# Kernel optimization log

Measured on AMD Instinct MI355X. Metric: run time of the kernel, lower is better.

## Reference

```python
import jax, jax.numpy as jnp
import numpy as np

OVERLAP_THRESHOLD = 0.5
NEG_POS_RATIO = 3
ALPHA = 1.0


def cxcy_to_xy(cxcy):
    return jnp.concatenate([cxcy[..., :2] - cxcy[..., 2:] / 2,
                            cxcy[..., :2] + cxcy[..., 2:] / 2], axis=-1)


def xy_to_cxcy(xy):
    return jnp.concatenate([(xy[..., :2] + xy[..., 2:]) / 2,
                            xy[..., 2:] - xy[..., :2]], axis=-1)


def cxcy_to_gcxgcy(cxcy, priors_cxcy):
    return jnp.concatenate([
        (cxcy[..., :2] - priors_cxcy[..., :2]) / (priors_cxcy[..., 2:] / 10.0),
        jnp.log(cxcy[..., 2:] / priors_cxcy[..., 2:]) * 5.0], axis=-1)


def jaccard(a, b):
    # a: [N,4] xy, b: [P,4] xy -> [N,P]
    lo = jnp.maximum(a[:, None, :2], b[None, :, :2])
    hi = jnp.minimum(a[:, None, 2:], b[None, :, 2:])
    inter = jnp.prod(jnp.clip(hi - lo, 0.0), axis=-1)  # [N,P]
    area_a = jnp.prod(a[:, 2:] - a[:, :2], axis=-1)  # [N]
    area_b = jnp.prod(b[:, 2:] - b[:, :2], axis=-1)  # [P]
    return inter / (area_a[:, None] + area_b[None, :] - inter)


def _match_one(boxes_i, labels_i, priors_cxcy, priors_xy):
    n_objects = boxes_i.shape[0]
    overlap = jaccard(boxes_i, priors_xy)  # [N,P]
    overlap_for_each_prior = overlap.max(axis=0)  # [P]
    object_for_each_prior = overlap.argmax(axis=0)  # [P]
    prior_for_each_object = overlap.argmax(axis=1)  # [N]
    # force each object to own its best prior
    object_for_each_prior = object_for_each_prior.at[prior_for_each_object].set(
        jnp.arange(n_objects))
    overlap_for_each_prior = overlap_for_each_prior.at[prior_for_each_object].set(1.0)
    labels_for_each_prior = labels_i[object_for_each_prior]
    labels_for_each_prior = jnp.where(overlap_for_each_prior < OVERLAP_THRESHOLD,
                                      0, labels_for_each_prior)
    matched = boxes_i[object_for_each_prior]  # [P,4]
    true_locs = cxcy_to_gcxgcy(xy_to_cxcy(matched), priors_cxcy)  # [P,4]
    return true_locs, labels_for_each_prior


def reference(predicted_locs, predicted_scores, boxes, labels, priors_cxcy):
    B, P, C = predicted_scores.shape
    priors_xy = cxcy_to_xy(priors_cxcy)
    true_locs, true_classes = jax.vmap(
        _match_one, in_axes=(0, 0, None, None))(boxes, labels, priors_cxcy, priors_xy)
    # true_locs: [B,P,4], true_classes: [B,P]
    positive = true_classes != 0  # [B,P]
    n_pos = positive.sum(axis=1)  # [B]
    n_pos_total = n_pos.sum()

    # SmoothL1 (beta=1, mean over selected elements = n_pos_total*4)
    d = predicted_locs - true_locs
    ad = jnp.abs(d)
    sl1 = jnp.where(ad < 1.0, 0.5 * d * d, ad - 0.5)  # [B,P,4]
    loc_loss = (sl1 * positive[..., None]).sum() / (n_pos_total.astype(jnp.float32) * 4.0)

    # per-prior cross-entropy
    logp = jax.nn.log_softmax(predicted_scores, axis=-1)  # [B,P,C]
    conf_all = -jnp.take_along_axis(logp, true_classes[..., None], axis=-1)[..., 0]  # [B,P]

    conf_pos_sum = jnp.where(positive, conf_all, 0.0).sum()
    conf_neg = jnp.where(positive, 0.0, conf_all)
    conf_neg_sorted = jnp.sort(conf_neg, axis=1)[:, ::-1]  # descending
    n_hard_neg = NEG_POS_RATIO * n_pos  # [B]
    rank = jnp.arange(P)[None, :]
    hard_neg_mask = rank < n_hard_neg[:, None]
    conf_hard_neg_sum = jnp.where(hard_neg_mask, conf_neg_sorted, 0.0).sum()

    conf_loss = (conf_hard_neg_sum + conf_pos_sum) / n_pos_total.astype(jnp.float32)
    return conf_loss + ALPHA * loc_loss


def setup_inputs() -> dict:
    key = jax.random.key(0)
    ks = jax.random.split(key, 7)
    B, P, C, N = 128, 8732, 21, 16
    predicted_locs = jax.random.normal(ks[0], (B, P, 4), dtype=jnp.float32)
    predicted_scores = jax.random.normal(ks[1], (B, P, C), dtype=jnp.float32)
    # valid xy boxes in [0,1]
    p1 = jax.random.uniform(ks[2], (B, N, 2)) * 0.85
    wh = jax.random.uniform(ks[3], (B, N, 2), minval=0.02, maxval=0.15)
    boxes = jnp.concatenate([p1, jnp.minimum(p1 + wh, 1.0)], axis=-1)
    labels = jax.random.randint(ks[4], (B, N), 1, C)
    cxcy = jax.random.uniform(ks[5], (P, 2))
    pwh = jax.random.uniform(ks[6], (P, 2), minval=0.05, maxval=0.5)
    priors_cxcy = jnp.concatenate([cxcy, pwh], axis=-1)
    return {"predicted_locs": predicted_locs, "predicted_scores": predicted_scores,
            "boxes": boxes, "labels": labels, "priors_cxcy": priors_cxcy}
```

## Files before the change

### kernel.cpp

```cpp
#include <hip/hip_runtime.h>


#define MAXN 16
#define MAXE 16

__device__ __forceinline__ float sl1f(float d) {
    float ad = fabsf(d);
    return ad < 1.0f ? 0.5f * d * d : ad - 0.5f;
}

__global__ __launch_bounds__(256) void k_bestprior(
    const float* __restrict__ boxes,
    const float* __restrict__ priors,
    int P, int N,
    int* __restrict__ pfo,
    int* __restrict__ npos)
{
    __shared__ float rv[4];
    __shared__ int   riq[4];
    const int id = blockIdx.x;
    const int tid = threadIdx.x;
    const int lane = tid & 63, wid = tid >> 6;

    if (tid == 0 && (id % N) == 0) npos[id / N] = 0;

    const float* bp = boxes + (size_t)id * 4;
    const float bx1 = bp[0], by1 = bp[1], bx2 = bp[2], by2 = bp[3];
    const float ba = (bx2 - bx1) * (by2 - by1);

    float v = -1.0f; int i = 0x7fffffff;
#pragma unroll 2
    for (int p = tid; p < P; p += 256) {
        float4 pr = ((const float4*)priors)[p];
        float px1 = pr.x - pr.z * 0.5f, py1 = pr.y - pr.w * 0.5f;
        float px2 = pr.x + pr.z * 0.5f, py2 = pr.y + pr.w * 0.5f;
        float parea = (px2 - px1) * (py2 - py1);
        float iw = fmaxf(fminf(bx2, px2) - fmaxf(bx1, px1), 0.0f);
        float ih = fmaxf(fminf(by2, py2) - fmaxf(by1, py1), 0.0f);
        float inter = iw * ih;
        float iou = inter / (ba + parea - inter);
        if (iou > v) { v = iou; i = p; }
    }
#pragma unroll
    for (int off = 32; off > 0; off >>= 1) {
        float ov = __shfl_down(v, off);
        int   oi = __shfl_down(i, off);
        if (ov > v || (ov == v && oi < i)) { v = ov; i = oi; }
    }
    if (lane == 0) { rv[wid] = v; riq[wid] = i; }
    __syncthreads();
    if (tid == 0) {
        for (int w = 1; w < 4; w++) {
            float ov = rv[w]; int oi = riq[w];
            if (ov > v || (ov == v && oi < i)) { v = ov; i = oi; }
        }
        pfo[id] = i;
    }
}

__global__ __launch_bounds__(256) void k_fused(
    const float* __restrict__ plocs,
    const float* __restrict__ scores,
    const float* __restrict__ boxes,
    const int*   __restrict__ labels,
    const float* __restrict__ priors,
    const int*   __restrict__ pfo,
    int P, int C, int N, int nchunk,
    float* __restrict__ conf_out,
    int*   __restrict__ npos,
    float* __restrict__ locpart,
    float* __restrict__ pospart)
{
    extern __shared__ float sh[];
    __shared__ float sx1[MAXN], sy1[MAXN], sx2[MAXN], sy2[MAXN], barea[MAXN];
    __shared__ int   blab[MAXN], spfo[MAXN];
    __shared__ float redf[4], redp[4];
    __shared__ int   redi[4];

    const int b = blockIdx.y;
    const int tid = threadIdx.x;
    const int lane = tid & 63, wid = tid >> 6;
    if (N > MAXN) N = MAXN;
    const int p0 = blockIdx.x * 256;
    const int rows = min(256, P - p0);

    if (tid < N) {
        const float* bp = boxes + ((size_t)b * N + tid) * 4;
        float x1 = bp[0], y1 = bp[1], x2 = bp[2], y2 = bp[3];
        sx1[tid] = x1; sy1[tid] = y1; sx2[tid] = x2; sy2[tid] = y2;
        barea[tid] = (x2 - x1) * (y2 - y1);
        blab[tid] = labels[(size_t)b * N + tid];
        spfo[tid] = pfo[b * N + tid];
    }

    {
        const size_t f4base = ((size_t)b * P + p0) * C / 4;
        const int f4cnt = (rows * C + 3) / 4;
        const float4* __restrict__ s4 = (const float4*)scores;
        for (int j = tid; j < f4cnt; j += 256)
            ((float4*)sh)[j] = s4[f4base + j];
    }
    __syncthreads();

    const int p = p0 + tid;
    float locs = 0.0f, posc = 0.0f, conf = 0.0f;
    int np = 0;
    if (p < P) {
        float4 pr = ((const float4*)priors)[p];
        float px1 = pr.x - pr.z * 0.5f, py1 = pr.y - pr.w * 0.5f;
        float px2 = pr.x + pr.z * 0.5f, py2 = pr.y + pr.w * 0.5f;
        float parea = (px2 - px1) * (py2 - py1);
        float best = -1.0f; int bestn = 0;
#pragma unroll
        for (int n = 0; n < MAXN; n++) {
            if (n < N) {
                float iw = fmaxf(fminf(sx2[n], px2) - fmaxf(sx1[n], px1), 0.0f);
                float ih = fmaxf(fminf(sy2[n], py2) - fmaxf(sy1[n], py1), 0.0f);
                float inter = iw * ih;
                float iou = inter / (barea[n] + parea - inter);
                if (iou > best) { best = iou; bestn = n; }
            }
        }
#pragma unroll
        for (int n = 0; n < MAXN; n++) {
            if (n < N && spfo[n] == p) { bestn = n; best = 1.0f; }
        }
        const int lab = (best < 0.5f) ? 0 : blab[bestn];

        const float* r = sh + tid * C;
        float m = -3.402823466e38f;
        for (int c = 0; c < C; c++) m = fmaxf(m, r[c]);
        float sum = 0.0f;
        for (int c = 0; c < C; c++) sum += __expf(r[c] - m);
        float ce = m + __logf(sum) - r[lab];

        if (lab != 0) {
            posc = ce; np = 1;
            int n = bestn;
            float cx = (sx1[n] + sx2[n]) * 0.5f, cy = (sy1[n] + sy2[n]) * 0.5f;
            float w = sx2[n] - sx1[n], h = sy2[n] - sy1[n];
            float g0 = (cx - pr.x) / (pr.z / 10.0f);
            float g1 = (cy - pr.y) / (pr.w / 10.0f);
            float g2 = logf(w / pr.z) * 5.0f;
            float g3 = logf(h / pr.w) * 5.0f;
            float4 pl = ((const float4*)plocs)[(size_t)b * P + p];
            locs = sl1f(pl.x - g0) + sl1f(pl.y - g1) + sl1f(pl.z - g2) + sl1f(pl.w - g3);
        } else {
            conf = ce;
        }
        conf_out[(size_t)b * P + p] = conf;
    }
#pragma unroll
    for (int off = 32; off > 0; off >>= 1) {
        locs += __shfl_down(locs, off);
        posc += __shfl_down(posc, off);
        np   += __shfl_down(np, off);
    }
    if (lane == 0) { redf[wid] = locs; redp[wid] = posc; redi[wid] = np; }
    __syncthreads();
    if (tid == 0) {
        float L = redf[0] + redf[1] + redf[2] + redf[3];
        float Pp = redp[0] + redp[1] + redp[2] + redp[3];
        int   c = redi[0] + redi[1] + redi[2] + redi[3];
        if (c) atomicAdd(&npos[b], c);
        locpart[b * nchunk + blockIdx.x] = L;
        pospart[b * nchunk + blockIdx.x] = Pp;
    }
}

__global__ __launch_bounds__(1024, 4) void k_hard(
    const float* __restrict__ conf,
    const int* __restrict__ npos,
    int P,
    float* __restrict__ hardsum)
{
    __shared__ int   redi[16 * 3];
    __shared__ float redf2[16];
    __shared__ int   redi2[16];
    const int b = blockIdx.x, tid = threadIdx.x;
    const int lane = tid & 63, wid = tid >> 6;
    const int nthr = blockDim.x, nw = nthr >> 6;
    const int ne = (P + nthr - 1) / nthr;
    long long kk = (long long)npos[b] * 3;
    int k = kk > P ? P : (int)kk;
    if (k <= 0) {
        if (tid == 0) hardsum[b] = 0.0f;
        return;
    }

    unsigned e[MAXE];
#pragma unroll
    for (int j = 0; j < MAXE; j++) {
        int p = j * nthr + tid;
        e[j] = (j < ne && p < P) ? __float_as_uint(conf[(size_t)b * P + p]) : 0u;
    }

    unsigned lo = 0u, hi = 0x7F800000u;
    while (lo < hi) {
        unsigned span = hi - lo;
        if (span >= 8) {
            unsigned q = span >> 2;
            unsigned m1 = lo + q, m2 = lo + 2 * q, m3 = lo + 3 * q;
            int c1 = 0, c2 = 0, c3 = 0;
#pragma unroll
            for (int j = 0; j < MAXE; j++) {
                if (j < ne) {
                    unsigned v = e[j];
                    c1 += (int)__popcll(__ballot(v >= m1));
                    c2 += (int)__popcll(__ballot(v >= m2));
                    c3 += (int)__popcll(__ballot(v >= m3));
                }
            }
            if (lane == 0) {
                redi[wid * 3 + 0] = c1; redi[wid * 3 + 1] = c2; redi[wid * 3 + 2] = c3;
            }
            __syncthreads();
            int C1 = 0, C2 = 0, C3 = 0;
            for (int w = 0; w < nw; w++) {
                C1 += redi[w * 3 + 0]; C2 += redi[w * 3 + 1]; C3 += redi[w * 3 + 2];
            }
            __syncthreads();
            if      (C3 >= k) lo = m3;
            else if (C2 >= k) { lo = m2; hi = m3 - 1; }
            else if (C1 >= k) { lo = m1; hi = m2 - 1; }
            else              hi = m1 - 1;
        } else {
            unsigned mid = lo + ((span + 1) >> 1);
            int c = 0;
#pragma unroll
            for (int j = 0; j < MAXE; j++)
                if (j < ne) c += (int)__popcll(__ballot(e[j] >= mid));
            if (lane == 0) redi[wid * 3] = c;
            __syncthreads();
            int Cc = 0;
            for (int w = 0; w < nw; w++) Cc += redi[w * 3];
            __syncthreads();
            if (Cc >= k) lo = mid; else hi = mid - 1;
        }
    }

    float t = __uint_as_float(lo);
    float sgt = 0.0f; int cgt = 0;
#pragma unroll
    for (int j = 0; j < MAXE; j++) {
        if (j < ne) {
            float v = __uint_as_float(e[j]);
            if (v > t) { sgt += v; cgt++; }
        }
    }
#pragma unroll
    for (int off = 32; off > 0; off >>= 1) {
        sgt += __shfl_down(sgt, off);
        cgt += __shfl_down(cgt, off);
    }
    if (lane == 0) { redf2[wid] = sgt; redi2[wid] = cgt; }
    __syncthreads();
    if (tid == 0) {
        float S = 0.0f; int Cg = 0;
        for (int w = 0; w < nw; w++) { S += redf2[w]; Cg += redi2[w]; }
        hardsum[b] = S + (float)(k - Cg) * t;
    }
}

__global__ __launch_bounds__(1024) void k_final(
    const int* __restrict__ npos, const float* __restrict__ locpart,
    const float* __restrict__ pospart, const float* __restrict__ hardsum,
    int B, int nloc, float* __restrict__ out)
{
    const int tid = threadIdx.x, lane = tid & 63, wid = tid >> 6;
    __shared__ float rf[3 * 16];
    __shared__ int   ri[16];
    float lp = 0, pp = 0, hp = 0; int np = 0;
    for (int i = tid; i < B; i += 1024) { np += npos[i]; hp += hardsum[i]; }
    for (int i = tid; i < nloc; i += 1024) { lp += locpart[i]; pp += pospart[i]; }
#pragma unroll
    for (int off = 32; off > 0; off >>= 1) {
        np += __shfl_down(np, off); lp += __shfl_down(lp, off);
        pp += __shfl_down(pp, off); hp += __shfl_down(hp, off);
    }
    if (lane == 0) { ri[wid] = np; rf[wid] = lp; rf[16 + wid] = pp; rf[32 + wid] = hp; }
    __syncthreads();
    if (tid == 0) {
        int nw = (int)(blockDim.x >> 6);
        float L = 0, Pp = 0, H = 0; int Np = 0;
        for (int w = 0; w < nw; w++) { Np += ri[w]; L += rf[w]; Pp += rf[16 + w]; H += rf[32 + w]; }
        float npf = (float)Np;
        out[0] = (H + Pp) / npf + L / (npf * 4.0f);
    }
}

extern "C" void kernel_launch(void* const* d_in, const int* in_sizes, int n_in,
                              void* d_out, int out_size, void* d_ws, size_t ws_size,
                              hipStream_t stream)
{
    const float* plocs  = (const float*)d_in[0];
    const float* scores = (const float*)d_in[1];
    const float* boxes  = (const float*)d_in[2];
    const int*   labels = (const int*)d_in[3];
    const float* priors = (const float*)d_in[4];

    int P = in_sizes[4] / 4;
    int B = in_sizes[0] / (P * 4);
    int C = in_sizes[1] / (in_sizes[0] / 4);
    int N = in_sizes[3] / B;
    int nchunk = (P + 255) / 256;
    int BN = B * N;

    char* w = (char*)d_ws;
    float* slot    = (float*)w;  w += (size_t)B * P * sizeof(float);
    int*   npos    = (int*)w;    w += (size_t)B * sizeof(int);
    int*   pfo     = (int*)w;    w += (size_t)BN * sizeof(int);
    float* locpart = (float*)w;  w += (size_t)B * nchunk * sizeof(float);
    float* pospart = (float*)w;  w += (size_t)B * nchunk * sizeof(float);
    float* hardsum = (float*)w;

    k_bestprior<<<BN, 256, 0, stream>>>(boxes, priors, P, N, pfo, npos);

    dim3 ga(nchunk, B);
    size_t smf = (size_t)256 * C * sizeof(float);
    k_fused<<<ga, 256, smf, stream>>>(plocs, scores, boxes, labels, priors, pfo,
                                      P, C, N, nchunk, slot, npos, locpart, pospart);

    k_hard<<<B, 1024, 0, stream>>>(slot, npos, P, hardsum);

    k_final<<<1, 1024, 0, stream>>>(npos, locpart, pospart, hardsum,
                                    B, B * nchunk, (float*)d_out);
}
```

Measured before the change: 221.4 us.

## Fold final reduction into hard-negative kernel via atomics; divide-free IoU comparisons

Removes the separate final reduction kernel. The fused kernel now atomically accumulates loc, positive-conf and positive-count totals into a small accumulator. The last block of the hard-negative kernel, detected with a ticket counter, computes the output. IoU argmax comparisons are rewritten as cross-multiplication to avoid divisions. This saves one launch and the divides, but adds about 4.4k float atomics on two addresses, which may contend, and gives nondeterministic summation order.

```diff
diff --git a/kernel.cpp b/kernel.cpp
--- a/kernel.cpp
+++ b/kernel.cpp
@@ -9,26 +9,28 @@
     return ad < 1.0f ? 0.5f * d * d : ad - 0.5f;
 }
 
-__global__ __launch_bounds__(256) void k_bestprior(
+__global__ __launch_bounds__(256) void k_pre(
     const float* __restrict__ boxes,
     const float* __restrict__ priors,
     int P, int N,
     int* __restrict__ pfo,
-    int* __restrict__ npos)
+    int* __restrict__ npos,
+    float* __restrict__ acc)
 {
-    __shared__ float rv[4];
-    __shared__ int   riq[4];
+    __shared__ float rin[4], run[4];
+    __shared__ int   rid[4];
     const int id = blockIdx.x;
     const int tid = threadIdx.x;
     const int lane = tid & 63, wid = tid >> 6;
 
     if (tid == 0 && (id % N) == 0) npos[id / N] = 0;
+    if (id == 0 && tid < 8) ((unsigned*)acc)[tid] = 0u;
 
     const float* bp = boxes + (size_t)id * 4;
     const float bx1 = bp[0], by1 = bp[1], bx2 = bp[2], by2 = bp[3];
     const float ba = (bx2 - bx1) * (by2 - by1);
 
-    float v = -1.0f; int i = 0x7fffffff;
+    float bi = -1.0f, bu = 1.0f; int idx = 0x7fffffff;
 #pragma unroll 2
     for (int p = tid; p < P; p += 256) {
         float4 pr = ((const float4*)priors)[p];
@@ -37,24 +39,27 @@
         float parea = (px2 - px1) * (py2 - py1);
         float iw = fmaxf(fminf(bx2, px2) - fmaxf(bx1, px1), 0.0f);
         float ih = fmaxf(fminf(by2, py2) - fmaxf(by1, py1), 0.0f);
-        float inter = iw * ih;
-        float iou = inter / (ba + parea - inter);
-        if (iou > v) { v = iou; i = p; }
+        float in = iw * ih;
+        float un = ba + parea - in;
+        if (in * bu > bi * un) { bi = in; bu = un; idx = p; }
     }
 #pragma unroll
     for (int off = 32; off > 0; off >>= 1) {
-        float ov = __shfl_down(v, off);
-        int   oi = __shfl_down(i, off);
-        if (ov > v || (ov == v && oi < i)) { v = ov; i = oi; }
-    }
-    if (lane == 0) { rv[wid] = v; riq[wid] = i; }
+        float oin = __shfl_down(bi, off);
+        float oun = __shfl_down(bu, off);
+        int   oid = __shfl_down(idx, off);
+        float a = oin * bu, c = bi * oun;
+        if (a > c || (a == c && oid < idx)) { bi = oin; bu = oun; idx = oid; }
+    }
+    if (lane == 0) { rin[wid] = bi; run[wid] = bu; rid[wid] = idx; }
     __syncthreads();
     if (tid == 0) {
         for (int w = 1; w < 4; w++) {
-            float ov = rv[w]; int oi = riq[w];
-            if (ov > v || (ov == v && oi < i)) { v = ov; i = oi; }
-        }
-        pfo[id] = i;
+            float oin = rin[w], oun = run[w]; int oid = rid[w];
+            float a = oin * bu, c = bi * oun;
+            if (a > c || (a == c && oid < idx)) { bi = oin; bu = oun; idx = oid; }
+        }
+        pfo[id] = idx;
     }
 }
 
@@ -65,11 +70,10 @@
     const int*   __restrict__ labels,
     const float* __restrict__ priors,
     const int*   __restrict__ pfo,
-    int P, int C, int N, int nchunk,
+    int P, int C, int N,
     float* __restrict__ conf_out,
     int*   __restrict__ npos,
-    float* __restrict__ locpart,
-    float* __restrict__ pospart)
+    float* __restrict__ acc)
 {
     extern __shared__ float sh[];
     __shared__ float sx1[MAXN], sy1[MAXN], sx2[MAXN], sy2[MAXN], barea[MAXN];
@@ -110,22 +114,22 @@
         float px1 = pr.x - pr.z * 0.5f, py1 = pr.y - pr.w * 0.5f;
         float px2 = pr.x + pr.z * 0.5f, py2 = pr.y + pr.w * 0.5f;
         float parea = (px2 - px1) * (py2 - py1);
-        float best = -1.0f; int bestn = 0;
+        float bi = -1.0f, bu = 1.0f; int bestn = 0;
 #pragma unroll
         for (int n = 0; n < MAXN; n++) {
             if (n < N) {
                 float iw = fmaxf(fminf(sx2[n], px2) - fmaxf(sx1[n], px1), 0.0f);
                 float ih = fmaxf(fminf(sy2[n], py2) - fmaxf(sy1[n], py1), 0.0f);
-                float inter = iw * ih;
-                float iou = inter / (barea[n] + parea - inter);
-                if (iou > best) { best = iou; bestn = n; }
+                float in = iw * ih;
+                float un = barea[n] + parea - in;
+                if (in * bu > bi * un) { bi = in; bu = un; bestn = n; }
             }
         }
 #pragma unroll
         for (int n = 0; n < MAXN; n++) {
-            if (n < N && spfo[n] == p) { bestn = n; best = 1.0f; }
-        }
-        const int lab = (best < 0.5f) ? 0 : blab[bestn];
+            if (n < N && spfo[n] == p) { bestn = n; bi = 1.0f; bu = 1.0f; }
+        }
+        const int lab = (bi < 0.5f * bu) ? 0 : blab[bestn];
 
         const float* r = sh + tid * C;
         float m = -3.402823466e38f;
@@ -162,9 +166,12 @@
         float L = redf[0] + redf[1] + redf[2] + redf[3];
         float Pp = redp[0] + redp[1] + redp[2] + redp[3];
         int   c = redi[0] + redi[1] + redi[2] + redi[3];
-        if (c) atomicAdd(&npos[b], c);
-        locpart[b * nchunk + blockIdx.x] = L;
-        pospart[b * nchunk + blockIdx.x] = Pp;
+        atomicAdd(&acc[0], L);
+        atomicAdd(&acc[1], Pp);
+        if (c) {
+            atomicAdd(&npos[b], c);
+            atomicAdd((int*)(acc + 3), c);
+        }
     }
 }
 
@@ -172,7 +179,8 @@
     const float* __restrict__ conf,
     const int* __restrict__ npos,
     int P,
-    float* __restrict__ hardsum)
+    float* __restrict__ acc,
+    float* __restrict__ out)
 {
     __shared__ int   redi[16 * 3];
     __shared__ float redf2[16];
@@ -183,109 +191,95 @@
     const int ne = (P + nthr - 1) / nthr;
     long long kk = (long long)npos[b] * 3;
     int k = kk > P ? P : (int)kk;
-    if (k <= 0) {
-        if (tid == 0) hardsum[b] = 0.0f;
-        return;
-    }
-
-    unsigned e[MAXE];
-#pragma unroll
-    for (int j = 0; j < MAXE; j++) {
-        int p = j * nthr + tid;
-        e[j] = (j < ne && p < P) ? __float_as_uint(conf[(size_t)b * P + p]) : 0u;
-    }
-
-    unsigned lo = 0u, hi = 0x7F800000u;
-    while (lo < hi) {
-        unsigned span = hi - lo;
-        if (span >= 8) {
-            unsigned q = span >> 2;
-            unsigned m1 = lo + q, m2 = lo + 2 * q, m3 = lo + 3 * q;
-            int c1 = 0, c2 = 0, c3 = 0;
-#pragma unroll
-            for (int j = 0; j < MAXE; j++) {
-                if (j < ne) {
-                    unsigned v = e[j];
-                    c1 += (int)__popcll(__ballot(v >= m1));
-                    c2 += (int)__popcll(__ballot(v >= m2));
-                    c3 += (int)__popcll(__ballot(v >= m3));
+
+    float S = 0.0f;
+    if (k > 0) {
+        unsigned e[MAXE];
+#pragma unroll
+        for (int j = 0; j < MAXE; j++) {
+            int p = j * nthr + tid;
+            e[j] = (j < ne && p < P) ? __float_as_uint(conf[(size_t)b * P + p]) : 0u;
+        }
+
+        unsigned lo = 0u, hi = 0x7F800000u;
+        while (lo < hi) {
+            unsigned span = hi - lo;
+            if (span >= 8) {
+                unsigned q = span >> 2;
+                unsigned m1 = lo + q, m2 = lo + 2 * q, m3 = lo + 3 * q;
+                int c1 = 0, c2 = 0, c3 = 0;
+#pragma unroll
+                for (int j = 0; j < MAXE; j++) {
+                    if (j < ne) {
+                        unsigned v = e[j];
+                        c1 += (int)__popcll(__ballot(v >= m1));
+                        c2 += (int)__popcll(__ballot(v >= m2));
+                        c3 += (int)__popcll(__ballot(v >= m3));
+                    }
                 }
+                if (lane == 0) {
+                    redi[wid * 3 + 0] = c1; redi[wid * 3 + 1] = c2; redi[wid * 3 + 2] = c3;
+                }
+                __syncthreads();
+                int C1 = 0, C2 = 0, C3 = 0;
+                for (int w = 0; w < nw; w++) {
+                    C1 += redi[w * 3 + 0]; C2 += redi[w * 3 + 1]; C3 += redi[w * 3 + 2];
+                }
+                __syncthreads();
+                if      (C3 >= k) lo = m3;
+                else if (C2 >= k) { lo = m2; hi = m3 - 1; }
+                else if (C1 >= k) { lo = m1; hi = m2 - 1; }
+                else              hi = m1 - 1;
+            } else {
+                unsigned mid = lo + ((span + 1) >> 1);
+                int c = 0;
+#pragma unroll
+                for (int j = 0; j < MAXE; j++)
+                    if (j < ne) c += (int)__popcll(__ballot(e[j] >= mid));
+                if (lane == 0) redi[wid * 3] = c;
+                __syncthreads();
+                int Cc = 0;
+                for (int w = 0; w < nw; w++) Cc += redi[w * 3];
+                __syncthreads();
+                if (Cc >= k) lo = mid; else hi = mid - 1;
             }
-            if (lane == 0) {
-                redi[wid * 3 + 0] = c1; redi[wid * 3 + 1] = c2; redi[wid * 3 + 2] = c3;
+        }
+
+        float t = __uint_as_float(lo);
+        float sgt = 0.0f; int cgt = 0;
+#pragma unroll
+        for (int j = 0; j < MAXE; j++) {
+            if (j < ne) {
+                float v = __uint_as_float(e[j]);
+                if (v > t) { sgt += v; cgt++; }
             }
-            __syncthreads();
-            int C1 = 0, C2 = 0, C3 = 0;
-            for (int w = 0; w < nw; w++) {
-                C1 += redi[w * 3 + 0]; C2 += redi[w * 3 + 1]; C3 += redi[w * 3 + 2];
-            }
-            __syncthreads();
-            if      (C3 >= k) lo = m3;
-            else if (C2 >= k) { lo = m2; hi = m3 - 1; }
-            else if (C1 >= k) { lo = m1; hi = m2 - 1; }
-            else              hi = m1 - 1;
-        } else {
-            unsigned mid = lo + ((span + 1) >> 1);
-            int c = 0;
-#pragma unroll
-            for (int j = 0; j < MAXE; j++)
-                if (j < ne) c += (int)__popcll(__ballot(e[j] >= mid));
-            if (lane == 0) redi[wid * 3] = c;
-            __syncthreads();
-            int Cc = 0;
-            for (int w = 0; w < nw; w++) Cc += redi[w * 3];
-            __syncthreads();
-            if (Cc >= k) lo = mid; else hi = mid - 1;
-        }
-    }
-
-    float t = __uint_as_float(lo);
-    float sgt = 0.0f; int cgt = 0;
-#pragma unroll
-    for (int j = 0; j < MAXE; j++) {
-        if (j < ne) {
-            float v = __uint_as_float(e[j]);
-            if (v > t) { sgt += v; cgt++; }
-        }
-    }
-#pragma unroll
-    for (int off = 32; off > 0; off >>= 1) {
-        sgt += __shfl_down(sgt, off);
-        cgt += __shfl_down(cgt, off);
-    }
-    if (lane == 0) { redf2[wid] = sgt; redi2[wid] = cgt; }
-    __syncthreads();
+        }
+#pragma unroll
+        for (int off = 32; off > 0; off >>= 1) {
+            sgt += __shfl_down(sgt, off);
+            cgt += __shfl_down(cgt, off);
+        }
+        if (lane == 0) { redf2[wid] = sgt; redi2[wid] = cgt; }
+        __syncthreads();
+        if (tid == 0) {
+            int Cg = 0;
+            for (int w = 0; w < nw; w++) { S += redf2[w]; Cg += redi2[w]; }
+            S += (float)(k - Cg) * t;
+        }
+    }
+
     if (tid == 0) {
-        float S = 0.0f; int Cg = 0;
-        for (int w = 0; w < nw; w++) { S += redf2[w]; Cg += redi2[w]; }
-        hardsum[b] = S + (float)(k - Cg) * t;
-    }
-}
-
-__global__ __launch_bounds__(1024) void k_final(
-    const int* __restrict__ npos, const float* __restrict__ locpart,
-    const float* __restrict__ pospart, const float* __restrict__ hardsum,
-    int B, int nloc, float* __restrict__ out)
-{
-    const int tid = threadIdx.x, lane = tid & 63, wid = tid >> 6;
-    __shared__ float rf[3 * 16];
-    __shared__ int   ri[16];
-    float lp = 0, pp = 0, hp = 0; int np = 0;
-    for (int i = tid; i < B; i += 1024) { np += npos[i]; hp += hardsum[i]; }
-    for (int i = tid; i < nloc; i += 1024) { lp += locpart[i]; pp += pospart[i]; }
-#pragma unroll
-    for (int off = 32; off > 0; off >>= 1) {
-        np += __shfl_down(np, off); lp += __shfl_down(lp, off);
-        pp += __shfl_down(pp, off); hp += __shfl_down(hp, off);
-    }
-    if (lane == 0) { ri[wid] = np; rf[wid] = lp; rf[16 + wid] = pp; rf[32 + wid] = hp; }
-    __syncthreads();
-    if (tid == 0) {
-        int nw = (int)(blockDim.x >> 6);
-        float L = 0, Pp = 0, H = 0; int Np = 0;
-        for (int w = 0; w < nw; w++) { Np += ri[w]; L += rf[w]; Pp += rf[16 + w]; H += rf[32 + w]; }
-        float npf = (float)Np;
-        out[0] = (H + Pp) / npf + L / (npf * 4.0f);
+        atomicAdd(&acc[2], S);
+        __threadfence();
+        unsigned tk = atomicAdd((unsigned*)(acc + 4), 1u);
+        if (tk == gridDim.x - 1) {
+            float loc  = atomicAdd(&acc[0], 0.0f);
+            float pos  = atomicAdd(&acc[1], 0.0f);
+            float hard = atomicAdd(&acc[2], 0.0f);
+            int   Np   = atomicAdd((int*)(acc + 3), 0);
+            float npf = (float)Np;
+            out[0] = (hard + pos) / npf + loc / (npf * 4.0f);
+        }
     }
 }
 
@@ -307,22 +301,18 @@
     int BN = B * N;
 
     char* w = (char*)d_ws;
-    float* slot    = (float*)w;  w += (size_t)B * P * sizeof(float);
-    int*   npos    = (int*)w;    w += (size_t)B * sizeof(int);
-    int*   pfo     = (int*)w;    w += (size_t)BN * sizeof(int);
-    float* locpart = (float*)w;  w += (size_t)B * nchunk * sizeof(float);
-    float* pospart = (float*)w;  w += (size_t)B * nchunk * sizeof(float);
-    float* hardsum = (float*)w;
-
-    k_bestprior<<<BN, 256, 0, stream>>>(boxes, priors, P, N, pfo, npos);
+    float* slot = (float*)w;  w += (size_t)B * P * sizeof(float);
+    int*   npos = (int*)w;    w += (size_t)B * sizeof(int);
+    int*   pfo  = (int*)w;    w += (size_t)BN * sizeof(int);
+    w = (char*)(((uintptr_t)w + 63) & ~(uintptr_t)63);
+    float* acc  = (float*)w;
+
+    k_pre<<<BN, 256, 0, stream>>>(boxes, priors, P, N, pfo, npos, acc);
 
     dim3 ga(nchunk, B);
     size_t smf = (size_t)256 * C * sizeof(float);
     k_fused<<<ga, 256, smf, stream>>>(plocs, scores, boxes, labels, priors, pfo,
-                                      P, C, N, nchunk, slot, npos, locpart, pospart);
-
-    k_hard<<<B, 1024, 0, stream>>>(slot, npos, P, hardsum);
-
-    k_final<<<1, 1024, 0, stream>>>(npos, locpart, pospart, hardsum,
-                                    B, B * nchunk, (float*)d_out);
-}
+                                      P, C, N, slot, npos, acc);
+
+    k_hard<<<B, 1024, 0, stream>>>(slot, npos, P, acc, (float*)d_out);
+}
```

New measurement: 324.8 us. 46.7% more time.
